# Performance work log

Hardware: AMD Instinct MI355X
Metric: run time of the kernel (lower is better)

## Reference

```python
import jax, jax.numpy as jnp
import numpy as np

B, N, D = 8, 2048, 768
H = 12
HD = D // H
W = 16          # window_size
HOP = 8         # hop_size
GB = N // 2 + 1   # global freq bins = 1025
LB = W // 2 + 1   # local freq bins = 9
NW = (N - W) // HOP + 1  # num windows = 255
EPS_LN = 1e-5


def setup_inputs() -> dict:
    key = jax.random.key(0)
    ks = jax.random.split(key, 12)
    s = 0.02
    return {
        "x": jax.random.normal(ks[0], (B, N, D), dtype=jnp.float32),
        "base_filter_global": jnp.ones((H, GB, 1), jnp.float32),
        "base_filter_local": jnp.ones((H, LB, 1), jnp.float32),
        "modrelu_bias_global": jnp.full((H, GB, 1), -0.1, jnp.float32),
        "modrelu_bias_local": jnp.full((H, LB, 1), -0.1, jnp.float32),
        "w1g": jax.random.normal(ks[1], (D, D), jnp.float32) * s,
        "b1g": jnp.zeros((D,), jnp.float32),
        "w2g": jax.random.normal(ks[2], (D, H * GB), jnp.float32) * s,
        "b2g": jnp.zeros((H * GB,), jnp.float32),
        "w1l": jax.random.normal(ks[3], (D, D), jnp.float32) * s,
        "b1l": jnp.zeros((D,), jnp.float32),
        "w2l": jax.random.normal(ks[4], (D, H * LB), jnp.float32) * s,
        "b2l": jnp.zeros((H * LB,), jnp.float32),
        "fusion_w": jax.random.normal(ks[5], (2,), jnp.float32) * 0.5,
        "ln_gamma": jnp.ones((D,), jnp.float32),
        "ln_beta": jnp.zeros((D,), jnp.float32),
    }


def _modrelu(z, bias):
    # modReLU: ReLU(|z| + b) * z / |z|  (|z| clamped at 1e-6 in denominator)
    a = jnp.abs(z)
    return z * (jax.nn.relu(a + bias) / jnp.maximum(a, 1e-6))


def _hann(w):
    # torch.hann_window default (periodic=True)
    n = jnp.arange(w, dtype=jnp.float32)
    return 0.5 * (1.0 - jnp.cos(2.0 * jnp.pi * n / w))


def reference(x, base_filter_global, base_filter_local, modrelu_bias_global,
              modrelu_bias_local, w1g, b1g, w2g, b2g, w1l, b1l, w2l, b2l,
              fusion_w, ln_gamma, ln_beta):
    b, n, d = x.shape
    x_heads = x.reshape(b, n, H, HD).transpose(0, 2, 1, 3)  # (B,H,N,hd)

    # ---- global branch ----
    Fg = jnp.fft.rfft(x_heads, axis=2, norm='ortho')  # (B,H,GB,hd) complex
    ctx = x.mean(axis=1)  # (B,D)
    mg = jnp.tanh(jax.nn.gelu(ctx @ w1g + b1g, approximate=False) @ w2g + b2g)
    mg = mg.reshape(b, H, GB, 1)
    Fg = Fg * (base_filter_global[None] + mg)
    Fg = _modrelu(Fg, modrelu_bias_global[None])
    x_global = jnp.fft.irfft(Fg, n=n, axis=2, norm='ortho')  # (B,H,N,hd)

    # ---- local (STFT) branch ----
    idx = jnp.arange(NW)[:, None] * HOP + jnp.arange(W)[None, :]  # (NW,W)
    x_win = x_heads[:, :, idx, :]  # (B,H,NW,W,hd)
    w = _hann(W)[None, None, None, :, None]
    x_win = x_win * w
    Fl = jnp.fft.rfft(x_win, axis=3, norm='ortho')  # (B,H,NW,LB,hd)
    ml = jnp.tanh(jax.nn.gelu(ctx @ w1l + b1l, approximate=False) @ w2l + b2l)
    ml = ml.reshape(b, H, 1, LB, 1)
    Fl = Fl * (base_filter_local[None, :, None] + ml)
    Fl = _modrelu(Fl, modrelu_bias_local[None, :, None])
    x_lwin = jnp.fft.irfft(Fl, n=W, axis=3, norm='ortho') * w  # (B,H,NW,W,hd)

    # vectorized overlap-add
    flat_idx = idx.reshape(-1)  # (NW*W,)
    x_local = jnp.zeros((b, H, n, HD), x.dtype).at[:, :, flat_idx, :].add(
        x_lwin.reshape(b, H, NW * W, HD))

    # ---- fuse + residual + layernorm ----
    fused = x_global * fusion_w[0] + x_local * fusion_w[1]  # Linear(2,1,bias=False)
    x_out = fused.transpose(0, 2, 1, 3).reshape(b, n, d)
    y = x + x_out  # dropout is identity at p=0 / eval
    mu = y.mean(axis=-1, keepdims=True)
    var = y.var(axis=-1, keepdims=True)
    return (y - mu) / jnp.sqrt(var + EPS_LN) * ln_gamma + ln_beta
```

## Files before the change

### kernel.cpp

```cpp
#include <hip/hip_runtime.h>
#include <math.h>

#define B_  8
#define N_  2048
#define D_  768
#define H_  12
#define HD_ 64
#define GB_ 1025
#define LB_ 9
#define NW_ 255

#define CBX(i) ((i) + ((i) >> 4))
#define TWX(i) ((i) + ((i) >> 4))

#define C1_ 0.92387953251128674f
#define S1_ 0.38268343236508978f
#define R2_ 0.70710678118654752f

#define FBF(i,k,wr,wi) { const float ar=yr[i],ai=yi[i],br=yr[k],bi=yi[k]; \
  yr[i]=ar+br; yi[i]=ai+bi; const float dr=ar-br, di=ai-bi; \
  yr[k]=fmaf(dr,wr,-(di*(wi))); yi[k]=fmaf(dr,wi,di*(wr)); }
#define FBF1(i,k) { const float ar=yr[i],ai=yi[i],br=yr[k],bi=yi[k]; \
  yr[i]=ar+br; yi[i]=ai+bi; yr[k]=ar-br; yi[k]=ai-bi; }
#define FBFmi(i,k) { const float ar=yr[i],ai=yi[i],br=yr[k],bi=yi[k]; \
  yr[i]=ar+br; yi[i]=ai+bi; yr[k]=ai-bi; yi[k]=br-ar; }

#define IBF(i,k,wr,wi) { const float br=yr[k],bi=yi[k]; \
  const float tr=fmaf(br,wr,-(bi*(wi))), ti=fmaf(br,wi,bi*(wr)); \
  yr[k]=yr[i]-tr; yi[k]=yi[i]-ti; yr[i]+=tr; yi[i]+=ti; }
#define IBF1(i,k) { const float tr=yr[k], ti=yi[k]; \
  yr[k]=yr[i]-tr; yi[k]=yi[i]-ti; yr[i]+=tr; yi[i]+=ti; }
#define IBFpi(i,k) { const float tr=-yi[k], ti=yr[k]; \
  yr[k]=yr[i]-tr; yi[k]=yi[i]-ti; yr[i]+=tr; yi[i]+=ti; }

__device__ __forceinline__ float2 cmulf(float2 a, float2 b) {
  return make_float2(fmaf(a.x, b.x, -(a.y*b.y)), fmaf(a.x, b.y, a.y*b.x));
}
__device__ __forceinline__ float2 cmulcf(float2 a, float2 b) {
  return make_float2(fmaf(a.x, b.x, a.y*b.y), fmaf(a.y, b.x, -(a.x*b.y)));
}
__device__ __forceinline__ float2 caddf(float2 a, float2 b){ return make_float2(a.x+b.x, a.y+b.y); }
__device__ __forceinline__ float2 csubf(float2 a, float2 b){ return make_float2(a.x-b.x, a.y-b.y); }
__device__ __forceinline__ float2 csqf(float2 a){ return make_float2(fmaf(a.x,a.x,-(a.y*a.y)), 2.0f*a.x*a.y); }

template<int S, int L>
__device__ __forceinline__ void fft_trip_fwd(float2* cb, const float2* tw, int j) {
  const int r    = j & (S-1);
  const int base = r + ((j >> L) << (L+3));
  float2 v[8];
  #pragma unroll
  for (int k = 0; k < 8; ++k) v[k] = cb[CBX(base + S*k)];
  const float2 w = tw[TWX(r * (256/S))];
  const float2 c8 = make_float2(R2_, -R2_);
  float2 W1[4];
  W1[0] = w;
  W1[1] = cmulf(w, c8);
  W1[2] = make_float2(w.y, -w.x);
  W1[3] = make_float2(W1[1].y, -W1[1].x);
  #pragma unroll
  for (int k = 0; k < 4; ++k) {
    const float2 u = v[k], t = v[k+4];
    v[k]   = caddf(u, t);
    v[k+4] = cmulf(csubf(u, t), W1[k]);
  }
  const float2 w2  = csqf(w);
  const float2 w2i = make_float2(w2.y, -w2.x);
  {
    float2 d;
    d = csubf(v[0], v[2]); v[0] = caddf(v[0], v[2]); v[2] = cmulf(d, w2);
    d = csubf(v[1], v[3]); v[1] = caddf(v[1], v[3]); v[3] = cmulf(d, w2i);
    d = csubf(v[4], v[6]); v[4] = caddf(v[4], v[6]); v[6] = cmulf(d, w2);
    d = csubf(v[5], v[7]); v[5] = caddf(v[5], v[7]); v[7] = cmulf(d, w2i);
  }
  const float2 w4 = csqf(w2);
  #pragma unroll
  for (int k = 0; k < 8; k += 2) {
    const float2 d = csubf(v[k], v[k+1]);
    v[k]   = caddf(v[k], v[k+1]);
    v[k+1] = cmulf(d, w4);
  }
  #pragma unroll
  for (int k = 0; k < 8; ++k) cb[CBX(base + S*k)] = v[k];
}

__device__ __forceinline__ void fft_trip4_fwd(float2* cb, int j) {
  const int base = j << 3;
  float2 v[8];
  #pragma unroll
  for (int k = 0; k < 8; ++k) v[k] = cb[CBX(base + k)];
  float2 d;
  d = csubf(v[0], v[2]); v[0] = caddf(v[0], v[2]); v[2] = d;
  d = csubf(v[1], v[3]); v[1] = caddf(v[1], v[3]); v[3] = make_float2(d.y, -d.x);
  d = csubf(v[4], v[6]); v[4] = caddf(v[4], v[6]); v[6] = d;
  d = csubf(v[5], v[7]); v[5] = caddf(v[5], v[7]); v[7] = make_float2(d.y, -d.x);
  #pragma unroll
  for (int k = 0; k < 8; k += 2) {
    d = csubf(v[k], v[k+1]);
    v[k]   = caddf(v[k], v[k+1]);
    v[k+1] = d;
  }
  #pragma unroll
  for (int k = 0; k < 8; ++k) cb[CBX(base + k)] = v[k];
}

__device__ __forceinline__ void fft_trip1_inv(float2* cb, int j) {
  const int base = j << 3;
  float2 v[8];
  #pragma unroll
  for (int k = 0; k < 8; ++k) v[k] = cb[CBX(base + k)];
  #pragma unroll
  for (int k = 0; k < 8; k += 2) {
    const float2 t = v[k+1];
    v[k+1] = csubf(v[k], t);
    v[k]   = caddf(v[k], t);
  }
  {
    float2 t;
    t = v[2];                              v[2] = csubf(v[0], t); v[0] = caddf(v[0], t);
    t = make_float2(-v[3].y, v[3].x);      v[3] = csubf(v[1], t); v[1] = caddf(v[1], t);
    t = v[6];                              v[6] = csubf(v[4], t); v[4] = caddf(v[4], t);
    t = make_float2(-v[7].y, v[7].x);      v[7] = csubf(v[5], t); v[5] = caddf(v[5], t);
  }
  #pragma unroll
  for (int k = 0; k < 8; ++k) cb[CBX(base + k)] = v[k];
}

template<int S, int L>
__device__ __forceinline__ void fft_trip_inv(float2* cb, const float2* tw, int j) {
  const int r    = j & (S-1);
  const int base = r + ((j >> L) << (L+3));
  float2 v[8];
  #pragma unroll
  for (int k = 0; k < 8; ++k) v[k] = cb[CBX(base + S*k)];
  const float2 w  = tw[TWX(r * (256/S))];
  const float2 w2 = csqf(w);
  const float2 w4 = csqf(w2);
  #pragma unroll
  for (int k = 0; k < 8; k += 2) {
    const float2 t = cmulcf(v[k+1], w4);
    v[k+1] = csubf(v[k], t);
    v[k]   = caddf(v[k], t);
  }
  {
    float2 t;
    t = cmulcf(v[2], w2);                          v[2] = csubf(v[0], t); v[0] = caddf(v[0], t);
    t = cmulcf(v[3], w2); t = make_float2(-t.y, t.x); v[3] = csubf(v[1], t); v[1] = caddf(v[1], t);
    t = cmulcf(v[6], w2);                          v[6] = csubf(v[4], t); v[4] = caddf(v[4], t);
    t = cmulcf(v[7], w2); t = make_float2(-t.y, t.x); v[7] = csubf(v[5], t); v[5] = caddf(v[5], t);
  }
  const float2 c8 = make_float2(R2_, -R2_);
  float2 W1[4];
  W1[0] = w;
  W1[1] = cmulf(w, c8);
  W1[2] = make_float2(w.y, -w.x);
  W1[3] = make_float2(W1[1].y, -W1[1].x);
  #pragma unroll
  for (int k = 0; k < 4; ++k) {
    const float2 t = cmulcf(v[k+4], W1[k]);
    v[k+4] = csubf(v[k], t);
    v[k]   = caddf(v[k], t);
  }
  #pragma unroll
  for (int k = 0; k < 8; ++k) cb[CBX(base + S*k)] = v[k];
}

__global__ __launch_bounds__(256) void k_ctx(const float* __restrict__ x,
                                             float* __restrict__ ctx) {
  const int b = blockIdx.x;
  const int nc = blockIdx.y;
  const int tid = threadIdx.x;
  const int n0 = nc * 64;
  for (int c = tid; c < D_; c += 256) {
    float s = 0.0f;
    #pragma unroll 4
    for (int n = 0; n < 64; ++n)
      s += x[((size_t)(b*N_ + n0 + n))*D_ + c];
    atomicAdd(&ctx[b*D_ + c], s);
  }
}

__global__ __launch_bounds__(256) void k_mlp1(
    const float* __restrict__ ctx,
    const float* __restrict__ w1g, const float* __restrict__ b1g,
    const float* __restrict__ w1l, const float* __restrict__ b1l,
    float* __restrict__ h1g, float* __restrict__ h1l) {
  __shared__ float hs[B_*D_];
  __shared__ float red[4][16][33];
  const int tid = threadIdx.x;
  const bool isl = (blockIdx.y != 0);
  const float* w1 = isl ? w1l : w1g;
  const float* b1 = isl ? b1l : b1g;
  float*       h1 = isl ? h1l : h1g;
  const int j0 = (int)blockIdx.x * 64;

  for (int i = tid; i < B_*D_; i += 256) hs[i] = ctx[i] * (1.0f/(float)N_);
  __syncthreads();

  const int jg    = tid & 15;
  const int slice = tid >> 4;
  const int j     = j0 + jg*4;
  float acc[8][4] = {};
  {
    const float4* w14 = (const float4*)w1;
    const int jc = j >> 2;
    const int i0 = slice*48;
    #pragma unroll 4
    for (int ii = 0; ii < 48; ++ii) {
      const int i = i0 + ii;
      const float4 w = w14[(size_t)i*192 + jc];
      #pragma unroll
      for (int b = 0; b < 8; ++b) {
        const float hv = hs[b*D_ + i];
        acc[b][0] = fmaf(hv, w.x, acc[b][0]);
        acc[b][1] = fmaf(hv, w.y, acc[b][1]);
        acc[b][2] = fmaf(hv, w.z, acc[b][2]);
        acc[b][3] = fmaf(hv, w.w, acc[b][3]);
      }
    }
  }
  #pragma unroll
  for (int b = 0; b < 8; ++b) {
    #pragma unroll
    for (int q = 0; q < 4; ++q) {
      float v = acc[b][q];
      v += __shfl_xor(v, 16, 64);
      v += __shfl_xor(v, 32, 64);
      acc[b][q] = v;
    }
  }
  const int wv = tid >> 6;
  if ((tid & 63) < 16) {
    #pragma unroll
    for (int b = 0; b < 8; ++b)
      #pragma unroll
      for (int q = 0; q < 4; ++q)
        red[wv][jg][b*4+q] = acc[b][q];
  }
  __syncthreads();
  for (int s = tid; s < 512; s += 256) {
    const int jg2 = s >> 5;
    const int v2  = s & 31;
    const int b   = v2 >> 2, q = v2 & 3;
    const int jo  = j0 + jg2*4 + q;
    const float sum = red[0][jg2][v2] + red[1][jg2][v2]
                    + red[2][jg2][v2] + red[3][jg2][v2];
    const float v = sum + b1[jo];
    h1[(size_t)b*D_ + jo] = 0.5f * v * (1.0f + erff(v * 0.70710678118654752f));
  }
}

__global__ __launch_bounds__(256) void k_mlp2(
    const float* __restrict__ h1g, const float* __restrict__ h1l,
    const float* __restrict__ w2g, const float* __restrict__ b2g,
    const float* __restrict__ w2l, const float* __restrict__ b2l,
    float* __restrict__ mg, float* __restrict__ ml) {
  __shared__ float hs[B_*D_];
  __shared__ float red[4][16][33];
  const int tid = threadIdx.x;
  const bool isg = (blockIdx.x < 193);
  const float* h1 = isg ? h1g : h1l;
  const float* w2 = isg ? w2g : w2l;
  const float* b2 = isg ? b2g : b2l;
  float*       mo = isg ? mg  : ml;
  const int Jmax = isg ? (H_*GB_) : (H_*LB_);
  const int j0   = isg ? (int)blockIdx.x*64 : ((int)blockIdx.x-193)*64;

  for (int i = tid; i < B_*D_; i += 256) hs[i] = h1[i];
  __syncthreads();

  const int jg    = tid & 15;
  const int slice = tid >> 4;
  const int j     = j0 + jg*4;
  float acc[8][4] = {};
  if (j < Jmax) {
    const float4* w24 = (const float4*)w2;
    const int jc   = j >> 2;
    const int rowq = Jmax >> 2;
    const int i0   = slice*48;
    #pragma unroll 4
    for (int ii = 0; ii < 48; ++ii) {
      const int i = i0 + ii;
      const float4 w = w24[(size_t)i*rowq + jc];
      #pragma unroll
      for (int b = 0; b < 8; ++b) {
        const float hv = hs[b*D_ + i];
        acc[b][0] = fmaf(hv, w.x, acc[b][0]);
        acc[b][1] = fmaf(hv, w.y, acc[b][1]);
        acc[b][2] = fmaf(hv, w.z, acc[b][2]);
        acc[b][3] = fmaf(hv, w.w, acc[b][3]);
      }
    }
  }
  #pragma unroll
  for (int b = 0; b < 8; ++b) {
    #pragma unroll
    for (int q = 0; q < 4; ++q) {
      float v = acc[b][q];
      v += __shfl_xor(v, 16, 64);
      v += __shfl_xor(v, 32, 64);
      acc[b][q] = v;
    }
  }
  const int wv = tid >> 6;
  if ((tid & 63) < 16) {
    #pragma unroll
    for (int b = 0; b < 8; ++b)
      #pragma unroll
      for (int q = 0; q < 4; ++q)
        red[wv][jg][b*4+q] = acc[b][q];
  }
  __syncthreads();
  for (int s = tid; s < 512; s += 256) {
    const int jg2 = s >> 5;
    const int v2  = s & 31;
    const int b   = v2 >> 2, q = v2 & 3;
    const int jo  = j0 + jg2*4 + q;
    if (jo < Jmax) {
      const float sum = red[0][jg2][v2] + red[1][jg2][v2]
                      + red[2][jg2][v2] + red[3][jg2][v2];
      mo[(size_t)b*Jmax + jo] = tanhf(sum + b2[jo]);
    }
  }
}

__global__ __launch_bounds__(256) void k_spectral(
    const float* __restrict__ x,
    const float* __restrict__ bfg, const float* __restrict__ bfl,
    const float* __restrict__ mbg, const float* __restrict__ mbl,
    const float* __restrict__ mg,  const float* __restrict__ ml,
    const float* __restrict__ fw,  float* __restrict__ fused) {
  __shared__ float2 cb[N_ + (N_>>4)];
  __shared__ float2 tw[256 + 16];
  __shared__ float  t1b[4][8], t2b[4][8];
  __shared__ float  lf[LB_], lb[LB_];

  const int tid = threadIdx.x;
  const int id  = blockIdx.x;
  const int v_  = (id & 7) * 384 + (id >> 3);
  const int dp  = v_ & 31;
  const int bh  = v_ >> 5;
  const int h   = bh % H_;
  const int b   = bh / H_;
  const int d   = dp * 2;
  const int c   = h*HD_ + d;
  const int col0 = bh*HD_ + d;

  {
    float s_, c_;
    sincospif(-(float)tid * (1.0f/1024.0f), &s_, &c_);
    tw[TWX(tid)] = make_float2(c_, s_);
  }
  if (tid < LB_) {
    lf[tid] = bfl[h*LB_ + tid] + ml[(size_t)b*(H_*LB_) + h*LB_ + tid];
    lb[tid] = mbl[h*LB_ + tid];
  }
  for (int n = tid; n < N_; n += 256) {
    const float2 v = *(const float2*)&x[((size_t)(b*N_ + n))*D_ + c];
    cb[CBX(n)] = v;
  }
  __syncthreads();

  const float HWIN[16] = {0.0f, 0.038060233744356624f, 0.14644660940672624f, 0.30865828381745508f,
                          0.5f, 0.69134171618254492f, 0.85355339059327376f, 0.96193976625564337f,
                          1.0f, 0.96193976625564337f, 0.85355339059327376f, 0.69134171618254492f,
                          0.5f, 0.30865828381745508f, 0.14644660940672624f, 0.038060233744356624f};
  float w1a[16], w2a[16];
  {
    const int j = tid;
    if (j < NW_) {
      float yr[16], yi[16];
      #pragma unroll
      for (int t = 0; t < 16; ++t) {
        const float2 v = cb[CBX(j*8 + t)];
        yr[t] = v.x * HWIN[t];
        yi[t] = v.y * HWIN[t];
      }
      FBF1(0,8); FBF(1,9,C1_,-S1_); FBF(2,10,R2_,-R2_); FBF(3,11,S1_,-C1_);
      FBFmi(4,12); FBF(5,13,-S1_,-C1_); FBF(6,14,-R2_,-R2_); FBF(7,15,-C1_,-S1_);
      FBF1(0,4); FBF(1,5,R2_,-R2_); FBFmi(2,6); FBF(3,7,-R2_,-R2_);
      FBF1(8,12); FBF(9,13,R2_,-R2_); FBFmi(10,14); FBF(11,15,-R2_,-R2_);
      FBF1(0,2); FBFmi(1,3); FBF1(4,6); FBFmi(5,7);
      FBF1(8,10); FBFmi(9,11); FBF1(12,14); FBFmi(13,15);
      FBF1(0,1); FBF1(2,3); FBF1(4,5); FBF1(6,7);
      FBF1(8,9); FBF1(10,11); FBF1(12,13); FBF1(14,15);
      {
        const int IA[9] = {0,8,4,12,2,10,6,14,1};
        const int IB[9] = {0,15,7,11,3,13,5,9,1};
        #pragma unroll
        for (int l = 0; l <= 8; ++l) {
          const int ia = IA[l], ib = IB[l];
          const float Zar=yr[ia], Zai=yi[ia], Zbr=yr[ib], Zbi=yi[ib];
          float f1r = 0.125f*(Zar+Zbr), f1i = 0.125f*(Zai-Zbi);
          float f2r = 0.125f*(Zai+Zbi), f2i = 0.125f*(Zbr-Zar);
          const float ft = lf[l], bs = lb[l];
          f1r *= ft; f1i *= ft; f2r *= ft; f2i *= ft;
          const float a1 = sqrtf(f1r*f1r + f1i*f1i);
          const float m1 = fmaxf(a1 + bs, 0.0f) / fmaxf(a1, 1e-6f);
          f1r *= m1; f1i *= m1;
          const float a2 = sqrtf(f2r*f2r + f2i*f2i);
          const float m2 = fmaxf(a2 + bs, 0.0f) / fmaxf(a2, 1e-6f);
          f2r *= m2; f2i *= m2;
          yr[ia] = f1r - f2i; yi[ia] = f1i + f2r;
          if (l >= 1 && l <= 7) { yr[ib] = f1r + f2i; yi[ib] = f2r - f1i; }
        }
      }
      IBF1(0,1); IBF1(2,3); IBF1(4,5); IBF1(6,7);
      IBF1(8,9); IBF1(10,11); IBF1(12,13); IBF1(14,15);
      IBF1(0,2); IBFpi(1,3); IBF1(4,6); IBFpi(5,7);
      IBF1(8,10); IBFpi(9,11); IBF1(12,14); IBFpi(13,15);
      IBF1(0,4); IBF(1,5,R2_,R2_); IBFpi(2,6); IBF(3,7,-R2_,R2_);
      IBF1(8,12); IBF(9,13,R2_,R2_); IBFpi(10,14); IBF(11,15,-R2_,R2_);
      IBF1(0,8); IBF(1,9,C1_,S1_); IBF(2,10,R2_,R2_); IBF(3,11,S1_,C1_);
      IBFpi(4,12); IBF(5,13,-S1_,C1_); IBF(6,14,-R2_,R2_); IBF(7,15,-C1_,S1_);
      #pragma unroll
      for (int t = 0; t < 16; ++t) {
        const float q = 0.25f * HWIN[t];
        w1a[t] = yr[t] * q;
        w2a[t] = yi[t] * q;
      }
    } else {
      #pragma unroll
      for (int t = 0; t < 16; ++t) { w1a[t] = 0.0f; w2a[t] = 0.0f; }
    }
  }
  const int lane = tid & 63, wvi = tid >> 6;
  if (lane == 63 && tid < NW_) {
    #pragma unroll
    for (int s = 0; s < 8; ++s) { t1b[wvi][s] = w1a[8+s]; t2b[wvi][s] = w2a[8+s]; }
  }
  __syncthreads();

  float r1[8], r2[8];
  #pragma unroll
  for (int s = 0; s < 8; ++s) {
    float p1 = __shfl_up(w1a[s+8], 1, 64);
    float p2 = __shfl_up(w2a[s+8], 1, 64);
    if (lane == 0) {
      p1 = wvi ? t1b[wvi-1][s] : 0.0f;
      p2 = wvi ? t2b[wvi-1][s] : 0.0f;
    }
    r1[s] = w1a[s] + p1;
    r2[s] = w2a[s] + p2;
  }

  fft_trip_fwd<256,8>(cb, tw, tid); __syncthreads();
  fft_trip_fwd< 32,5>(cb, tw, tid); __syncthreads();
  fft_trip_fwd<  4,2>(cb, tw, tid); __syncthreads();
  fft_trip4_fwd(cb, tid);           __syncthreads();

  const float fsc = 0.022097086912079610f;
  {
    const float* mgp = mg + (size_t)b*(H_*GB_) + h*GB_;
    const float* bfp = bfg + h*GB_;
    const float* mbp = mbg + h*GB_;
    for (int k = tid; k < 1024; k += 256) {
      if (k == 0) {
        float2 Z0 = cb[CBX(0)], Zn = cb[CBX(1)];
        float g1 = Z0.x * fsc, g2 = Z0.y * fsc;
        {
          const float filt = bfp[0] + mgp[0], bias = mbp[0];
          g1 *= filt; g2 *= filt;
          float a1 = fabsf(g1); g1 *= fmaxf(a1 + bias, 0.0f) / fmaxf(a1, 1e-6f);
          float a2 = fabsf(g2); g2 *= fmaxf(a2 + bias, 0.0f) / fmaxf(a2, 1e-6f);
        }
        cb[CBX(0)] = make_float2(g1, g2);
        float n1 = Zn.x * fsc, n2 = Zn.y * fsc;
        {
          const float filt = bfp[1024] + mgp[1024], bias = mbp[1024];
          n1 *= filt; n2 *= filt;
          float a1 = fabsf(n1); n1 *= fmaxf(a1 + bias, 0.0f) / fmaxf(a1, 1e-6f);
          float a2 = fabsf(n2); n2 *= fmaxf(a2 + bias, 0.0f) / fmaxf(a2, 1e-6f);
        }
        cb[CBX(1)] = make_float2(n1, n2);
      } else {
        const int ik  = (int)(__brev((unsigned)k) >> 21);
        const int imk = (int)(__brev((unsigned)(2048 - k)) >> 21);
        const float2 Za = cb[CBX(ik)], Zb = cb[CBX(imk)];
        const float hs_ = 0.5f * fsc;
        float f1r = (Za.x + Zb.x) * hs_, f1i = (Za.y - Zb.y) * hs_;
        float f2r = (Za.y + Zb.y) * hs_, f2i = (Zb.x - Za.x) * hs_;
        const float filt = bfp[k] + mgp[k], bias = mbp[k];
        f1r *= filt; f1i *= filt; f2r *= filt; f2i *= filt;
        const float a1 = sqrtf(f1r*f1r + f1i*f1i);
        const float s1 = fmaxf(a1 + bias, 0.0f) / fmaxf(a1, 1e-6f);
        f1r *= s1; f1i *= s1;
        const float a2 = sqrtf(f2r*f2r + f2i*f2i);
        const float s2 = fmaxf(a2 + bias, 0.0f) / fmaxf(a2, 1e-6f);
        f2r *= s2; f2i *= s2;
        cb[CBX(ik)]  = make_float2(f1r - f2i, f1i + f2r);
        cb[CBX(imk)] = make_float2(f1r + f2i, f2r - f1i);
      }
    }
  }
  __syncthreads();

  fft_trip1_inv(cb, tid);           __syncthreads();
  fft_trip_inv<  4,2>(cb, tw, tid); __syncthreads();
  fft_trip_inv< 32,5>(cb, tw, tid); __syncthreads();
  fft_trip_inv<256,8>(cb, tw, tid); __syncthreads();

  const float fw1v = fw[1];
  const float fwg  = fw[0] * fsc;
  float* f0 = fused + (size_t)col0 * N_;
  float* f1p = f0 + N_;
  const int n0 = tid * 8;
  float v0[8], v1[8];
  #pragma unroll
  for (int s = 0; s < 8; ++s) {
    const float2 g = cb[CBX(n0 + s)];
    v0[s] = fwg * g.x + fw1v * r1[s];
    v1[s] = fwg * g.y + fw1v * r2[s];
  }
  *(float4*)&f0[n0]    = make_float4(v0[0], v0[1], v0[2], v0[3]);
  *(float4*)&f0[n0+4]  = make_float4(v0[4], v0[5], v0[6], v0[7]);
  *(float4*)&f1p[n0]   = make_float4(v1[0], v1[1], v1[2], v1[3]);
  *(float4*)&f1p[n0+4] = make_float4(v1[4], v1[5], v1[6], v1[7]);
}

__global__ __launch_bounds__(256) void k_ln(const float* __restrict__ x,
                                            const float* __restrict__ fused,
                                            const float* __restrict__ gamma,
                                            const float* __restrict__ beta,
                                            float* __restrict__ out) {
  __shared__ float yt[16*776];
  __shared__ float mus[16], rsd[16];
  const int bi = blockIdx.x;
  const int b  = bi >> 7;
  const int n0 = (bi & 127) * 16;
  const int tid = threadIdx.x;

  {
    const float4* x4 = (const float4*)(x + ((size_t)(b*N_ + n0))*D_);
    for (int i = tid; i < 16*D_/4; i += 256) {
      const int nn = i / 192, r = i - nn*192;
      const float4 v = x4[i];
      float* yp = &yt[nn*776 + r*4];
      yp[0] = v.x; yp[1] = v.y; yp[2] = v.z; yp[3] = v.w;
    }
  }
  __syncthreads();
  {
    const float4* fu4 = (const float4*)fused;
    for (int i = tid; i < 16*D_/4; i += 256) {
      const int cc = i >> 2, q = (i & 3) * 4;
      const float4 g = fu4[(((size_t)(b*D_ + cc))*N_ + n0)/4 + (i & 3)];
      yt[(q+0)*776 + cc] += g.x;
      yt[(q+1)*776 + cc] += g.y;
      yt[(q+2)*776 + cc] += g.z;
      yt[(q+3)*776 + cc] += g.w;
    }
  }
  __syncthreads();
  const int nn = tid >> 4, cl = tid & 15;
  float s1 = 0.0f, s2 = 0.0f;
  for (int c = cl; c < D_; c += 16) {
    const float v = yt[nn*776 + c];
    s1 += v; s2 += v*v;
  }
  #pragma unroll
  for (int m = 8; m >= 1; m >>= 1) {
    s1 += __shfl_xor(s1, m, 16);
    s2 += __shfl_xor(s2, m, 16);
  }
  if (cl == 0) {
    const float mu  = s1 * (1.0f/(float)D_);
    const float var = s2 * (1.0f/(float)D_) - mu*mu;
    mus[nn] = mu;
    rsd[nn] = rsqrtf(var + 1e-5f);
  }
  __syncthreads();
  {
    float4* o4 = (float4*)(out + ((size_t)(b*N_ + n0))*D_);
    const float4* g4 = (const float4*)gamma;
    const float4* be4 = (const float4*)beta;
    for (int i = tid; i < 16*D_/4; i += 256) {
      const int nn2 = i / 192, r = i - nn2*192;
      const float mu = mus[nn2], rs = rsd[nn2];
      const float4 gm = g4[r], bt = be4[r];
      const float* yp = &yt[nn2*776 + r*4];
      float4 o;
      o.x = (yp[0] - mu) * rs * gm.x + bt.x;
      o.y = (yp[1] - mu) * rs * gm.y + bt.y;
      o.z = (yp[2] - mu) * rs * gm.z + bt.z;
      o.w = (yp[3] - mu) * rs * gm.w + bt.w;
      o4[i] = o;
    }
  }
}

extern "C" void kernel_launch(void* const* d_in, const int* in_sizes, int n_in,
                              void* d_out, int out_size, void* d_ws, size_t ws_size,
                              hipStream_t stream) {
  const float* x   = (const float*)d_in[0];
  const float* bfg = (const float*)d_in[1];
  const float* bfl = (const float*)d_in[2];
  const float* mbg = (const float*)d_in[3];
  const float* mbl = (const float*)d_in[4];
  const float* w1g = (const float*)d_in[5];
  const float* b1g = (const float*)d_in[6];
  const float* w2g = (const float*)d_in[7];
  const float* b2g = (const float*)d_in[8];
  const float* w1l = (const float*)d_in[9];
  const float* b1l = (const float*)d_in[10];
  const float* w2l = (const float*)d_in[11];
  const float* b2l = (const float*)d_in[12];
  const float* fw  = (const float*)d_in[13];
  const float* gam = (const float*)d_in[14];
  const float* bet = (const float*)d_in[15];
  float* out = (float*)d_out;

  float* ws    = (float*)d_ws;
  float* ctx   = ws;
  float* h1g   = ws + 6144;
  float* h1l   = ws + 12288;
  float* mg    = ws + 18432;
  float* ml    = ws + 116832;
  float* fused = ws + 117696;

  hipMemsetAsync(ctx, 0, (size_t)B_*D_*sizeof(float), stream);
  k_ctx<<<dim3(B_, 32), 256, 0, stream>>>(x, ctx);
  k_mlp1<<<dim3(12, 2), 256, 0, stream>>>(ctx, w1g, b1g, w1l, b1l, h1g, h1l);
  k_mlp2<<<195, 256, 0, stream>>>(h1g, h1l, w2g, b2g, w2l, b2l, mg, ml);
  k_spectral<<<B_*H_*32, 256, 0, stream>>>(x, bfg, bfl, mbg, mbl, mg, ml, fw, fused);
  k_ln<<<B_*N_/16, 256, 0, stream>>>(x, fused, gam, bet, out);
}
```

Baseline: 297.7 us.

## Process four head-dim columns per spectral block with float4 FFT buffers

The spectral kernel now handles four columns per block (two packed complex FFTs) instead of two, using float4 shared-memory elements and halving the grid. Each column pair reuses the same twiddles and barriers, and global loads become 16-byte. It also swaps the modReLU divide and sqrt for the hardware rcp and sqrt builtins. The cost is a larger shared-memory footprint (about 35 KB for cb), more registers per thread, and fewer blocks, so occupancy may drop.

```diff
diff --git a/kernel.cpp b/kernel.cpp
--- a/kernel.cpp
+++ b/kernel.cpp
@@ -36,18 +36,42 @@
 __device__ __forceinline__ float2 cmulf(float2 a, float2 b) {
   return make_float2(fmaf(a.x, b.x, -(a.y*b.y)), fmaf(a.x, b.y, a.y*b.x));
 }
-__device__ __forceinline__ float2 cmulcf(float2 a, float2 b) {
-  return make_float2(fmaf(a.x, b.x, a.y*b.y), fmaf(a.y, b.x, -(a.x*b.y)));
-}
-__device__ __forceinline__ float2 caddf(float2 a, float2 b){ return make_float2(a.x+b.x, a.y+b.y); }
-__device__ __forceinline__ float2 csubf(float2 a, float2 b){ return make_float2(a.x-b.x, a.y-b.y); }
 __device__ __forceinline__ float2 csqf(float2 a){ return make_float2(fmaf(a.x,a.x,-(a.y*a.y)), 2.0f*a.x*a.y); }
 
+__device__ __forceinline__ float4 dadd(float4 a, float4 b){ return make_float4(a.x+b.x,a.y+b.y,a.z+b.z,a.w+b.w); }
+__device__ __forceinline__ float4 dsub(float4 a, float4 b){ return make_float4(a.x-b.x,a.y-b.y,a.z-b.z,a.w-b.w); }
+__device__ __forceinline__ float4 dmul(float4 a, float2 w){
+  return make_float4(fmaf(a.x,w.x,-(a.y*w.y)), fmaf(a.x,w.y,a.y*w.x),
+                     fmaf(a.z,w.x,-(a.w*w.y)), fmaf(a.z,w.y,a.w*w.x));
+}
+__device__ __forceinline__ float4 dmulc(float4 a, float2 w){
+  return make_float4(fmaf(a.x,w.x,a.y*w.y), fmaf(a.y,w.x,-(a.x*w.y)),
+                     fmaf(a.z,w.x,a.w*w.y), fmaf(a.w,w.x,-(a.z*w.y)));
+}
+__device__ __forceinline__ float4 dmuli(float4 a){
+  return make_float4(a.y, -a.x, a.w, -a.z);
+}
+__device__ __forceinline__ float4 dmulpi(float4 a){
+  return make_float4(-a.y, a.x, -a.w, a.z);
+}
+
+__device__ __forceinline__ void mr2(float& ar, float& ai, float filt, float bias){
+  ar *= filt; ai *= filt;
+  const float a = __builtin_amdgcn_sqrtf(fmaf(ar,ar,ai*ai));
+  const float s = fmaxf(a + bias, 0.0f) * __builtin_amdgcn_rcpf(fmaxf(a, 1e-6f));
+  ar *= s; ai *= s;
+}
+__device__ __forceinline__ void mr1(float& v, float filt, float bias){
+  v *= filt;
+  const float a = fabsf(v);
+  v *= fmaxf(a + bias, 0.0f) * __builtin_amdgcn_rcpf(fmaxf(a, 1e-6f));
+}
+
 template<int S, int L>
-__device__ __forceinline__ void fft_trip_fwd(float2* cb, const float2* tw, int j) {
+__device__ __forceinline__ void fft_trip_fwd(float4* cb, const float2* tw, int j) {
   const int r    = j & (S-1);
   const int base = r + ((j >> L) << (L+3));
-  float2 v[8];
+  float4 v[8];
   #pragma unroll
   for (int k = 0; k < 8; ++k) v[k] = cb[CBX(base + S*k)];
   const float2 w = tw[TWX(r * (256/S))];
@@ -59,77 +83,77 @@
   W1[3] = make_float2(W1[1].y, -W1[1].x);
   #pragma unroll
   for (int k = 0; k < 4; ++k) {
-    const float2 u = v[k], t = v[k+4];
-    v[k]   = caddf(u, t);
-    v[k+4] = cmulf(csubf(u, t), W1[k]);
+    const float4 u = v[k], t = v[k+4];
+    v[k]   = dadd(u, t);
+    v[k+4] = dmul(dsub(u, t), W1[k]);
   }
   const float2 w2  = csqf(w);
   const float2 w2i = make_float2(w2.y, -w2.x);
   {
-    float2 d;
-    d = csubf(v[0], v[2]); v[0] = caddf(v[0], v[2]); v[2] = cmulf(d, w2);
-    d = csubf(v[1], v[3]); v[1] = caddf(v[1], v[3]); v[3] = cmulf(d, w2i);
-    d = csubf(v[4], v[6]); v[4] = caddf(v[4], v[6]); v[6] = cmulf(d, w2);
-    d = csubf(v[5], v[7]); v[5] = caddf(v[5], v[7]); v[7] = cmulf(d, w2i);
+    float4 d;
+    d = dsub(v[0], v[2]); v[0] = dadd(v[0], v[2]); v[2] = dmul(d, w2);
+    d = dsub(v[1], v[3]); v[1] = dadd(v[1], v[3]); v[3] = dmul(d, w2i);
+    d = dsub(v[4], v[6]); v[4] = dadd(v[4], v[6]); v[6] = dmul(d, w2);
+    d = dsub(v[5], v[7]); v[5] = dadd(v[5], v[7]); v[7] = dmul(d, w2i);
   }
   const float2 w4 = csqf(w2);
   #pragma unroll
   for (int k = 0; k < 8; k += 2) {
-    const float2 d = csubf(v[k], v[k+1]);
-    v[k]   = caddf(v[k], v[k+1]);
-    v[k+1] = cmulf(d, w4);
+    const float4 d = dsub(v[k], v[k+1]);
+    v[k]   = dadd(v[k], v[k+1]);
+    v[k+1] = dmul(d, w4);
   }
   #pragma unroll
   for (int k = 0; k < 8; ++k) cb[CBX(base + S*k)] = v[k];
 }
 
-__device__ __forceinline__ void fft_trip4_fwd(float2* cb, int j) {
+__device__ __forceinline__ void fft_trip4_fwd(float4* cb, int j) {
   const int base = j << 3;
-  float2 v[8];
+  float4 v[8];
   #pragma unroll
   for (int k = 0; k < 8; ++k) v[k] = cb[CBX(base + k)];
-  float2 d;
-  d = csubf(v[0], v[2]); v[0] = caddf(v[0], v[2]); v[2] = d;
-  d = csubf(v[1], v[3]); v[1] = caddf(v[1], v[3]); v[3] = make_float2(d.y, -d.x);
-  d = csubf(v[4], v[6]); v[4] = caddf(v[4], v[6]); v[6] = d;
-  d = csubf(v[5], v[7]); v[5] = caddf(v[5], v[7]); v[7] = make_float2(d.y, -d.x);
+  float4 d;
+  d = dsub(v[0], v[2]); v[0] = dadd(v[0], v[2]); v[2] = d;
+  d = dsub(v[1], v[3]); v[1] = dadd(v[1], v[3]); v[3] = dmuli(d);
+  d = dsub(v[4], v[6]); v[4] = dadd(v[4], v[6]); v[6] = d;
+  d = dsub(v[5], v[7]); v[5] = dadd(v[5], v[7]); v[7] = dmuli(d);
   #pragma unroll
   for (int k = 0; k < 8; k += 2) {
-    d = csubf(v[k], v[k+1]);
-    v[k]   = caddf(v[k], v[k+1]);
+    d = dsub(v[k], v[k+1]);
+    v[k]   = dadd(v[k], v[k+1]);
     v[k+1] = d;
   }
   #pragma unroll
   for (int k = 0; k < 8; ++k) cb[CBX(base + k)] = v[k];
 }
 
-__device__ __forceinline__ void fft_trip1_inv(float2* cb, int j) {
+__device__ __forceinline__ void fft_trip1_inv(float4* cb, int j) {
   const int base = j << 3;
-  float2 v[8];
+  float4 v[8];
   #pragma unroll
   for (int k = 0; k < 8; ++k) v[k] = cb[CBX(base + k)];
   #pragma unroll
   for (int k = 0; k < 8; k += 2) {
-    const float2 t = v[k+1];
-    v[k+1] = csubf(v[k], t);
-    v[k]   = caddf(v[k], t);
-  }
-  {
-    float2 t;
-    t = v[2];                              v[2] = csubf(v[0], t); v[0] = caddf(v[0], t);
-    t = make_float2(-v[3].y, v[3].x);      v[3] = csubf(v[1], t); v[1] = caddf(v[1], t);
-    t = v[6];                              v[6] = csubf(v[4], t); v[4] = caddf(v[4], t);
-    t = make_float2(-v[7].y, v[7].x);      v[7] = csubf(v[5], t); v[5] = caddf(v[5], t);
+    const float4 t = v[k+1];
+    v[k+1] = dsub(v[k], t);
+    v[k]   = dadd(v[k], t);
+  }
+  {
+    float4 t;
+    t = v[2];          v[2] = dsub(v[0], t); v[0] = dadd(v[0], t);
+    t = dmulpi(v[3]);  v[3] = dsub(v[1], t); v[1] = dadd(v[1], t);
+    t = v[6];          v[6] = dsub(v[4], t); v[4] = dadd(v[4], t);
+    t = dmulpi(v[7]);  v[7] = dsub(v[5], t); v[5] = dadd(v[5], t);
   }
   #pragma unroll
   for (int k = 0; k < 8; ++k) cb[CBX(base + k)] = v[k];
 }
 
 template<int S, int L>
-__device__ __forceinline__ void fft_trip_inv(float2* cb, const float2* tw, int j) {
+__device__ __forceinline__ void fft_trip_inv(float4* cb, const float2* tw, int j) {
   const int r    = j & (S-1);
   const int base = r + ((j >> L) << (L+3));
-  float2 v[8];
+  float4 v[8];
   #pragma unroll
   for (int k = 0; k < 8; ++k) v[k] = cb[CBX(base + S*k)];
   const float2 w  = tw[TWX(r * (256/S))];
@@ -137,16 +161,16 @@
   const float2 w4 = csqf(w2);
   #pragma unroll
   for (int k = 0; k < 8; k += 2) {
-    const float2 t = cmulcf(v[k+1], w4);
-    v[k+1] = csubf(v[k], t);
-    v[k]   = caddf(v[k], t);
-  }
-  {
-    float2 t;
-    t = cmulcf(v[2], w2);                          v[2] = csubf(v[0], t); v[0] = caddf(v[0], t);
-    t = cmulcf(v[3], w2); t = make_float2(-t.y, t.x); v[3] = csubf(v[1], t); v[1] = caddf(v[1], t);
-    t = cmulcf(v[6], w2);                          v[6] = csubf(v[4], t); v[4] = caddf(v[4], t);
-    t = cmulcf(v[7], w2); t = make_float2(-t.y, t.x); v[7] = csubf(v[5], t); v[5] = caddf(v[5], t);
+    const float4 t = dmulc(v[k+1], w4);
+    v[k+1] = dsub(v[k], t);
+    v[k]   = dadd(v[k], t);
+  }
+  {
+    float4 t;
+    t = dmulc(v[2], w2);          v[2] = dsub(v[0], t); v[0] = dadd(v[0], t);
+    t = dmulpi(dmulc(v[3], w2));  v[3] = dsub(v[1], t); v[1] = dadd(v[1], t);
+    t = dmulc(v[6], w2);          v[6] = dsub(v[4], t); v[4] = dadd(v[4], t);
+    t = dmulpi(dmulc(v[7], w2));  v[7] = dsub(v[5], t); v[5] = dadd(v[5], t);
   }
   const float2 c8 = make_float2(R2_, -R2_);
   float2 W1[4];
@@ -156,12 +180,87 @@
   W1[3] = make_float2(W1[1].y, -W1[1].x);
   #pragma unroll
   for (int k = 0; k < 4; ++k) {
-    const float2 t = cmulcf(v[k+4], W1[k]);
-    v[k+4] = csubf(v[k], t);
-    v[k]   = caddf(v[k], t);
+    const float4 t = dmulc(v[k+4], W1[k]);
+    v[k+4] = dsub(v[k], t);
+    v[k]   = dadd(v[k], t);
   }
   #pragma unroll
   for (int k = 0; k < 8; ++k) cb[CBX(base + S*k)] = v[k];
+}
+
+template<int HALF>
+__device__ __forceinline__ void local_path(const float4* cb, const float* lf, const float* lb,
+                                           int tid, float* w1a, float* w2a) {
+  const float HWIN[16] = {0.0f, 0.038060233744356624f, 0.14644660940672624f, 0.30865828381745508f,
+                          0.5f, 0.69134171618254492f, 0.85355339059327376f, 0.96193976625564337f,
+                          1.0f, 0.96193976625564337f, 0.85355339059327376f, 0.69134171618254492f,
+                          0.5f, 0.30865828381745508f, 0.14644660940672624f, 0.038060233744356624f};
+  if (tid < NW_) {
+    float yr[16], yi[16];
+    #pragma unroll
+    for (int t = 0; t < 16; ++t) {
+      const float4 v = cb[CBX(tid*8 + t)];
+      yr[t] = (HALF ? v.z : v.x) * HWIN[t];
+      yi[t] = (HALF ? v.w : v.y) * HWIN[t];
+    }
+    FBF1(0,8); FBF(1,9,C1_,-S1_); FBF(2,10,R2_,-R2_); FBF(3,11,S1_,-C1_);
+    FBFmi(4,12); FBF(5,13,-S1_,-C1_); FBF(6,14,-R2_,-R2_); FBF(7,15,-C1_,-S1_);
+    FBF1(0,4); FBF(1,5,R2_,-R2_); FBFmi(2,6); FBF(3,7,-R2_,-R2_);
+    FBF1(8,12); FBF(9,13,R2_,-R2_); FBFmi(10,14); FBF(11,15,-R2_,-R2_);
+    FBF1(0,2); FBFmi(1,3); FBF1(4,6); FBFmi(5,7);
+    FBF1(8,10); FBFmi(9,11); FBF1(12,14); FBFmi(13,15);
+    FBF1(0,1); FBF1(2,3); FBF1(4,5); FBF1(6,7);
+    FBF1(8,9); FBF1(10,11); FBF1(12,13); FBF1(14,15);
+    {
+      const int IA[9] = {0,8,4,12,2,10,6,14,1};
+      const int IB[9] = {0,15,7,11,3,13,5,9,1};
+      #pragma unroll
+      for (int l = 0; l <= 8; ++l) {
+        const int ia = IA[l], ib = IB[l];
+        const float Zar=yr[ia], Zai=yi[ia], Zbr=yr[ib], Zbi=yi[ib];
+        float f1r = 0.125f*(Zar+Zbr), f1i = 0.125f*(Zai-Zbi);
+        float f2r = 0.125f*(Zai+Zbi), f2i = 0.125f*(Zbr-Zar);
+        const float ft = lf[l], bs = lb[l];
+        mr2(f1r, f1i, ft, bs);
+        mr2(f2r, f2i, ft, bs);
+        yr[ia] = f1r - f2i; yi[ia] = f1i + f2r;
+        if (l >= 1 && l <= 7) { yr[ib] = f1r + f2i; yi[ib] = f2r - f1i; }
+      }
+    }
+    IBF1(0,1); IBF1(2,3); IBF1(4,5); IBF1(6,7);
+    IBF1(8,9); IBF1(10,11); IBF1(12,13); IBF1(14,15);
+    IBF1(0,2); IBFpi(1,3); IBF1(4,6); IBFpi(5,7);
+    IBF1(8,10); IBFpi(9,11); IBF1(12,14); IBFpi(13,15);
+    IBF1(0,4); IBF(1,5,R2_,R2_); IBFpi(2,6); IBF(3,7,-R2_,R2_);
+    IBF1(8,12); IBF(9,13,R2_,R2_); IBFpi(10,14); IBF(11,15,-R2_,R2_);
+    IBF1(0,8); IBF(1,9,C1_,S1_); IBF(2,10,R2_,R2_); IBF(3,11,S1_,C1_);
+    IBFpi(4,12); IBF(5,13,-S1_,C1_); IBF(6,14,-R2_,R2_); IBF(7,15,-C1_,S1_);
+    #pragma unroll
+    for (int t = 0; t < 16; ++t) {
+      const float q = 0.25f * HWIN[t];
+      w1a[t] = yr[t] * q;
+      w2a[t] = yi[t] * q;
+    }
+  } else {
+    #pragma unroll
+    for (int t = 0; t < 16; ++t) { w1a[t] = 0.0f; w2a[t] = 0.0f; }
+  }
+}
+
+__device__ __forceinline__ void combine_oa(const float* w1a, const float* w2a,
+                                           const float (*t1)[8], const float (*t2)[8],
+                                           int lane, int wvi, float* r1, float* r2) {
+  #pragma unroll
+  for (int s = 0; s < 8; ++s) {
+    float p1 = __shfl_up(w1a[s+8], 1, 64);
+    float p2 = __shfl_up(w2a[s+8], 1, 64);
+    if (lane == 0) {
+      p1 = wvi ? t1[wvi-1][s] : 0.0f;
+      p2 = wvi ? t2[wvi-1][s] : 0.0f;
+    }
+    r1[s] = w1a[s] + p1;
+    r2[s] = w2a[s] + p2;
+  }
 }
 
 __global__ __launch_bounds__(256) void k_ctx(const float* __restrict__ x,
@@ -329,19 +428,19 @@
     const float* __restrict__ mbg, const float* __restrict__ mbl,
     const float* __restrict__ mg,  const float* __restrict__ ml,
     const float* __restrict__ fw,  float* __restrict__ fused) {
-  __shared__ float2 cb[N_ + (N_>>4)];
+  __shared__ float4 cb[N_ + (N_>>4)];
   __shared__ float2 tw[256 + 16];
-  __shared__ float  t1b[4][8], t2b[4][8];
+  __shared__ float  t1b[2][4][8], t2b[2][4][8];
   __shared__ float  lf[LB_], lb[LB_];
 
   const int tid = threadIdx.x;
   const int id  = blockIdx.x;
-  const int v_  = (id & 7) * 384 + (id >> 3);
-  const int dp  = v_ & 31;
-  const int bh  = v_ >> 5;
+  const int v_  = (id & 7) * 192 + (id >> 3);
+  const int dq  = v_ & 15;
+  const int bh  = v_ >> 4;
   const int h   = bh % H_;
   const int b   = bh / H_;
-  const int d   = dp * 2;
+  const int d   = dq * 4;
   const int c   = h*HD_ + d;
   const int col0 = bh*HD_ + d;
 
@@ -355,92 +454,31 @@
     lb[tid] = mbl[h*LB_ + tid];
   }
   for (int n = tid; n < N_; n += 256) {
-    const float2 v = *(const float2*)&x[((size_t)(b*N_ + n))*D_ + c];
-    cb[CBX(n)] = v;
-  }
-  __syncthreads();
-
-  const float HWIN[16] = {0.0f, 0.038060233744356624f, 0.14644660940672624f, 0.30865828381745508f,
-                          0.5f, 0.69134171618254492f, 0.85355339059327376f, 0.96193976625564337f,
-                          1.0f, 0.96193976625564337f, 0.85355339059327376f, 0.69134171618254492f,
-                          0.5f, 0.30865828381745508f, 0.14644660940672624f, 0.038060233744356624f};
-  float w1a[16], w2a[16];
-  {
-    const int j = tid;
-    if (j < NW_) {
-      float yr[16], yi[16];
+    cb[CBX(n)] = *(const float4*)&x[((size_t)(b*N_ + n))*D_ + c];
+  }
+  __syncthreads();
+
+  const int lane = tid & 63, wvi = tid >> 6;
+  float r1[8], r2[8], r3[8], r4[8];
+  {
+    float w1a[16], w2a[16];
+    local_path<0>(cb, lf, lb, tid, w1a, w2a);
+    if (lane == 63 && tid < NW_) {
       #pragma unroll
-      for (int t = 0; t < 16; ++t) {
-        const float2 v = cb[CBX(j*8 + t)];
-        yr[t] = v.x * HWIN[t];
-        yi[t] = v.y * HWIN[t];
-      }
-      FBF1(0,8); FBF(1,9,C1_,-S1_); FBF(2,10,R2_,-R2_); FBF(3,11,S1_,-C1_);
-      FBFmi(4,12); FBF(5,13,-S1_,-C1_); FBF(6,14,-R2_,-R2_); FBF(7,15,-C1_,-S1_);
-      FBF1(0,4); FBF(1,5,R2_,-R2_); FBFmi(2,6); FBF(3,7,-R2_,-R2_);
-      FBF1(8,12); FBF(9,13,R2_,-R2_); FBFmi(10,14); FBF(11,15,-R2_,-R2_);
-      FBF1(0,2); FBFmi(1,3); FBF1(4,6); FBFmi(5,7);
-      FBF1(8,10); FBFmi(9,11); FBF1(12,14); FBFmi(13,15);
-      FBF1(0,1); FBF1(2,3); FBF1(4,5); FBF1(6,7);
-      FBF1(8,9); FBF1(10,11); FBF1(12,13); FBF1(14,15);
-      {
-        const int IA[9] = {0,8,4,12,2,10,6,14,1};
-        const int IB[9] = {0,15,7,11,3,13,5,9,1};
-        #pragma unroll
-        for (int l = 0; l <= 8; ++l) {
-          const int ia = IA[l], ib = IB[l];
-          const float Zar=yr[ia], Zai=yi[ia], Zbr=yr[ib], Zbi=yi[ib];
-          float f1r = 0.125f*(Zar+Zbr), f1i = 0.125f*(Zai-Zbi);
-          float f2r = 0.125f*(Zai+Zbi), f2i = 0.125f*(Zbr-Zar);
-          const float ft = lf[l], bs = lb[l];
-          f1r *= ft; f1i *= ft; f2r *= ft; f2i *= ft;
-          const float a1 = sqrtf(f1r*f1r + f1i*f1i);
-          const float m1 = fmaxf(a1 + bs, 0.0f) / fmaxf(a1, 1e-6f);
-          f1r *= m1; f1i *= m1;
-          const float a2 = sqrtf(f2r*f2r + f2i*f2i);
-          const float m2 = fmaxf(a2 + bs, 0.0f) / fmaxf(a2, 1e-6f);
-          f2r *= m2; f2i *= m2;
-          yr[ia] = f1r - f2i; yi[ia] = f1i + f2r;
-          if (l >= 1 && l <= 7) { yr[ib] = f1r + f2i; yi[ib] = f2r - f1i; }
-        }
-      }
-      IBF1(0,1); IBF1(2,3); IBF1(4,5); IBF1(6,7);
-      IBF1(8,9); IBF1(10,11); IBF1(12,13); IBF1(14,15);
-      IBF1(0,2); IBFpi(1,3); IBF1(4,6); IBFpi(5,7);
-      IBF1(8,10); IBFpi(9,11); IBF1(12,14); IBFpi(13,15);
-      IBF1(0,4); IBF(1,5,R2_,R2_); IBFpi(2,6); IBF(3,7,-R2_,R2_);
-      IBF1(8,12); IBF(9,13,R2_,R2_); IBFpi(10,14); IBF(11,15,-R2_,R2_);
-      IBF1(0,8); IBF(1,9,C1_,S1_); IBF(2,10,R2_,R2_); IBF(3,11,S1_,C1_);
-      IBFpi(4,12); IBF(5,13,-S1_,C1_); IBF(6,14,-R2_,R2_); IBF(7,15,-C1_,S1_);
+      for (int s = 0; s < 8; ++s) { t1b[0][wvi][s] = w1a[8+s]; t2b[0][wvi][s] = w2a[8+s]; }
+    }
+    __syncthreads();
+    combine_oa(w1a, w2a, t1b[0], t2b[0], lane, wvi, r1, r2);
+  }
+  {
+    float w1a[16], w2a[16];
+    local_path<1>(cb, lf, lb, tid, w1a, w2a);
+    if (lane == 63 && tid < NW_) {
       #pragma unroll
-      for (int t = 0; t < 16; ++t) {
-        const float q = 0.25f * HWIN[t];
-        w1a[t] = yr[t] * q;
-        w2a[t] = yi[t] * q;
-      }
-    } else {
-      #pragma unroll
-      for (int t = 0; t < 16; ++t) { w1a[t] = 0.0f; w2a[t] = 0.0f; }
-    }
-  }
-  const int lane = tid & 63, wvi = tid >> 6;
-  if (lane == 63 && tid < NW_) {
-    #pragma unroll
-    for (int s = 0; s < 8; ++s) { t1b[wvi][s] = w1a[8+s]; t2b[wvi][s] = w2a[8+s]; }
-  }
-  __syncthreads();
-
-  float r1[8], r2[8];
-  #pragma unroll
-  for (int s = 0; s < 8; ++s) {
-    float p1 = __shfl_up(w1a[s+8], 1, 64);
-    float p2 = __shfl_up(w2a[s+8], 1, 64);
-    if (lane == 0) {
-      p1 = wvi ? t1b[wvi-1][s] : 0.0f;
-      p2 = wvi ? t2b[wvi-1][s] : 0.0f;
-    }
-    r1[s] = w1a[s] + p1;
-    r2[s] = w2a[s] + p2;
+      for (int s = 0; s < 8; ++s) { t1b[1][wvi][s] = w1a[8+s]; t2b[1][wvi][s] = w2a[8+s]; }
+    }
+    __syncthreads();
+    combine_oa(w1a, w2a, t1b[1], t2b[1], lane, wvi, r3, r4);
   }
 
   fft_trip_fwd<256,8>(cb, tw, tid); __syncthreads();
@@ -455,40 +493,31 @@
     const float* mbp = mbg + h*GB_;
     for (int k = tid; k < 1024; k += 256) {
       if (k == 0) {
-        float2 Z0 = cb[CBX(0)], Zn = cb[CBX(1)];
-        float g1 = Z0.x * fsc, g2 = Z0.y * fsc;
-        {
-          const float filt = bfp[0] + mgp[0], bias = mbp[0];
-          g1 *= filt; g2 *= filt;
-          float a1 = fabsf(g1); g1 *= fmaxf(a1 + bias, 0.0f) / fmaxf(a1, 1e-6f);
-          float a2 = fabsf(g2); g2 *= fmaxf(a2 + bias, 0.0f) / fmaxf(a2, 1e-6f);
-        }
-        cb[CBX(0)] = make_float2(g1, g2);
-        float n1 = Zn.x * fsc, n2 = Zn.y * fsc;
-        {
-          const float filt = bfp[1024] + mgp[1024], bias = mbp[1024];
-          n1 *= filt; n2 *= filt;
-          float a1 = fabsf(n1); n1 *= fmaxf(a1 + bias, 0.0f) / fmaxf(a1, 1e-6f);
-          float a2 = fabsf(n2); n2 *= fmaxf(a2 + bias, 0.0f) / fmaxf(a2, 1e-6f);
-        }
-        cb[CBX(1)] = make_float2(n1, n2);
+        float4 Z0 = cb[CBX(0)], Zn = cb[CBX(1)];
+        const float f0t = bfp[0] + mgp[0],     b0 = mbp[0];
+        const float fnt = bfp[1024] + mgp[1024], bn = mbp[1024];
+        float a0 = Z0.x*fsc, a1 = Z0.y*fsc, a2 = Z0.z*fsc, a3 = Z0.w*fsc;
+        mr1(a0, f0t, b0); mr1(a1, f0t, b0); mr1(a2, f0t, b0); mr1(a3, f0t, b0);
+        cb[CBX(0)] = make_float4(a0, a1, a2, a3);
+        float n0v = Zn.x*fsc, n1v = Zn.y*fsc, n2v = Zn.z*fsc, n3v = Zn.w*fsc;
+        mr1(n0v, fnt, bn); mr1(n1v, fnt, bn); mr1(n2v, fnt, bn); mr1(n3v, fnt, bn);
+        cb[CBX(1)] = make_float4(n0v, n1v, n2v, n3v);
       } else {
         const int ik  = (int)(__brev((unsigned)k) >> 21);
         const int imk = (int)(__brev((unsigned)(2048 - k)) >> 21);
-        const float2 Za = cb[CBX(ik)], Zb = cb[CBX(imk)];
+        const float4 Za = cb[CBX(ik)], Zb = cb[CBX(imk)];
         const float hs_ = 0.5f * fsc;
+        const float filt = bfp[k] + mgp[k], bias = mbp[k];
         float f1r = (Za.x + Zb.x) * hs_, f1i = (Za.y - Zb.y) * hs_;
         float f2r = (Za.y + Zb.y) * hs_, f2i = (Zb.x - Za.x) * hs_;
-        const float filt = bfp[k] + mgp[k], bias = mbp[k];
-        f1r *= filt; f1i *= filt; f2r *= filt; f2i *= filt;
-        const float a1 = sqrtf(f1r*f1r + f1i*f1i);
-        const float s1 = fmaxf(a1 + bias, 0.0f) / fmaxf(a1, 1e-6f);
-        f1r *= s1; f1i *= s1;
-        const float a2 = sqrtf(f2r*f2r + f2i*f2i);
-        const float s2 = fmaxf(a2 + bias, 0.0f) / fmaxf(a2, 1e-6f);
-        f2r *= s2; f2i *= s2;
-        cb[CBX(ik)]  = make_float2(f1r - f2i, f1i + f2r);
-        cb[CBX(imk)] = make_float2(f1r + f2i, f2r - f1i);
+        mr2(f1r, f1i, filt, bias);
+        mr2(f2r, f2i, filt, bias);
+        float g1r = (Za.z + Zb.z) * hs_, g1i = (Za.w - Zb.w) * hs_;
+        float g2r = (Za.w + Zb.w) * hs_, g2i = (Zb.z - Za.z) * hs_;
+        mr2(g1r, g1i, filt, bias);
+        mr2(g2r, g2i, filt, bias);
+        cb[CBX(ik)]  = make_float4(f1r - f2i, f1i + f2r, g1r - g2i, g1i + g2r);
+        cb[CBX(imk)] = make_float4(f1r + f2i, f2r - f1i, g1r + g2i, g2r - g1i);
       }
     }
   }
@@ -503,18 +532,26 @@
   const float fwg  = fw[0] * fsc;
   float* f0 = fused + (size_t)col0 * N_;
   float* f1p = f0 + N_;
+  float* f2p = f0 + 2*N_;
+  float* f3p = f0 + 3*N_;
   const int n0 = tid * 8;
-  float v0[8], v1[8];
+  float v0[8], v1[8], v2[8], v3[8];
   #pragma unroll
   for (int s = 0; s < 8; ++s) {
-    const float2 g = cb[CBX(n0 + s)];
+    const float4 g = cb[CBX(n0 + s)];
     v0[s] = fwg * g.x + fw1v * r1[s];
     v1[s] = fwg * g.y + fw1v * r2[s];
+    v2[s] = fwg * g.z + fw1v * r3[s];
+    v3[s] = fwg * g.w + fw1v * r4[s];
   }
   *(float4*)&f0[n0]    = make_float4(v0[0], v0[1], v0[2], v0[3]);
   *(float4*)&f0[n0+4]  = make_float4(v0[4], v0[5], v0[6], v0[7]);
   *(float4*)&f1p[n0]   = make_float4(v1[0], v1[1], v1[2], v1[3]);
   *(float4*)&f1p[n0+4] = make_float4(v1[4], v1[5], v1[6], v1[7]);
+  *(float4*)&f2p[n0]   = make_float4(v2[0], v2[1], v2[2], v2[3]);
+  *(float4*)&f2p[n0+4] = make_float4(v2[4], v2[5], v2[6], v2[7]);
+  *(float4*)&f3p[n0]   = make_float4(v3[0], v3[1], v3[2], v3[3]);
+  *(float4*)&f3p[n0+4] = make_float4(v3[4], v3[5], v3[6], v3[7]);
 }
 
 __global__ __launch_bounds__(256) void k_ln(const float* __restrict__ x,
@@ -621,6 +658,6 @@
   k_ctx<<<dim3(B_, 32), 256, 0, stream>>>(x, ctx);
   k_mlp1<<<dim3(12, 2), 256, 0, stream>>>(ctx, w1g, b1g, w1l, b1l, h1g, h1l);
   k_mlp2<<<195, 256, 0, stream>>>(h1g, h1l, w2g, b2g, w2l, b2l, mg, ml);
-  k_spectral<<<B_*H_*32, 256, 0, stream>>>(x, bfg, bfl, mbg, mbl, mg, ml, fw, fused);
+  k_spectral<<<B_*H_*16, 256, 0, stream>>>(x, bfg, bfl, mbg, mbl, mg, ml, fw, fused);
   k_ln<<<B_*N_/16, 256, 0, stream>>>(x, fused, gam, bet, out);
 }
```

Result: faster. 290.0 us (-2.6%).
